# Kernel tuning notes

Measured on AMD Instinct MI355X. Metric: run time of the kernel, lower is better.

Reference implementation:

```python
import jax, jax.numpy as jnp
import numpy as np

NEG_SLOPE = 0.01  # torch LeakyReLU default
BN_EPS = 1e-5     # torch BatchNorm1d default


def _bn(x, g, b):
    # training-mode batch norm over the node axis
    m = jnp.mean(x, axis=0)
    v = jnp.var(x, axis=0)
    return g * (x - m) * jax.lax.rsqrt(v + BN_EPS) + b


def _lrelu(x):
    return jax.nn.leaky_relu(x, NEG_SLOPE)


def setup_inputs() -> dict:
    key = jax.random.key(0)
    N, E, W, D = 100_000, 1_600_000, 32, 10
    ks = iter(jax.random.split(key, 64))

    def w(shape):
        fan_in = shape[-2] if len(shape) >= 2 else shape[-1]
        return (jax.random.normal(next(ks), shape, jnp.float32) / np.sqrt(fan_in)).astype(jnp.float32)

    inp = {}
    inp["x"] = jax.random.normal(next(ks), (N, 1), jnp.float32)
    inp["col_e_idx"] = jax.random.randint(next(ks), (2, E), 0, N, dtype=jnp.int32)
    # init_node_feature_trans: MLP 1 -> [32] -> 32, LeakyReLU, batch_norm=True
    inp["Wi0"] = w((1, W)); inp["bi0"] = jnp.zeros(W); inp["gi0"] = jnp.ones(W); inp["bei0"] = jnp.zeros(W)
    inp["Wi1"] = w((W, W)); inp["bi1"] = jnp.zeros(W); inp["gi1"] = jnp.ones(W); inp["bei1"] = jnp.zeros(W)
    # 10 CollConv layers (identical dims -> stacked params)
    inp["Wm"] = w((D, W, W)); inp["bm"] = jnp.zeros((D, W)); inp["gm"] = jnp.ones((D, W)); inp["bem"] = jnp.zeros((D, W))
    inp["Wu"] = w((D, 2 * W, W)); inp["bu"] = jnp.zeros((D, W)); inp["gu"] = jnp.ones((D, W)); inp["beu"] = jnp.zeros((D, W))
    # final_mlp: 32 -> 256 -> 128 -> 64 -> 32 (LeakyReLU, no BN), then 32 -> 1 sigmoid
    inp["Wf0"] = w((W, 256)); inp["bf0"] = jnp.zeros(256)
    inp["Wf1"] = w((256, 128)); inp["bf1"] = jnp.zeros(128)
    inp["Wf2"] = w((128, 64)); inp["bf2"] = jnp.zeros(64)
    inp["Wf3"] = w((64, W)); inp["bf3"] = jnp.zeros(W)
    inp["Wo"] = w((W, 1)); inp["bo"] = jnp.zeros(1)
    return inp


def reference(x, col_e_idx, Wi0, bi0, gi0, bei0, Wi1, bi1, gi1, bei1,
              Wm, bm, gm, bem, Wu, bu, gu, beu,
              Wf0, bf0, Wf1, bf1, Wf2, bf2, Wf3, bf3, Wo, bo):
    N = x.shape[0]
    D = Wm.shape[0]
    src, dst = col_e_idx[0], col_e_idx[1]

    # init node-feature MLP (Linear -> BN -> LeakyReLU, twice)
    h = _lrelu(_bn(x @ Wi0 + bi0, gi0, bei0))
    h = _lrelu(_bn(h @ Wi1 + bi1, gi1, bei1))

    feats = [h]  # middle_features[0]
    for i in range(D):  # fixed small depth -> python loop is fine
        # CollConv: node-wise message transform, edge gather, scatter-sum, update
        msg = _lrelu(_bn(h @ Wm[i] + bm[i], gm[i], bem[i]))      # [N, W]
        agg = jax.ops.segment_sum(msg[src], dst, num_segments=N)  # [N, W]
        h = _lrelu(_bn(jnp.concatenate([h, agg], axis=-1) @ Wu[i] + bu[i], gu[i], beu[i]))
        if i - 2 >= 0:  # residual_skip_num = 2
            h = h + feats[i - 2]
        feats.append(h)

    # final MLP (no BN) + sigmoid head
    h = _lrelu(h @ Wf0 + bf0)
    h = _lrelu(h @ Wf1 + bf1)
    h = _lrelu(h @ Wf2 + bf2)
    h = _lrelu(h @ Wf3 + bf3)
    return jax.nn.sigmoid(h @ Wo + bo)  # [N, 1]
```

## Files before the change

kernel.cpp:

```cpp
#include <hip/hip_runtime.h>
#include <hip/hip_bf16.h>

#define NN 100000
#define NEDGE 1600000
#define NV (NN*32)
#define NEG 0.01f
#define EPS 1e-5f
#define NBLK 391
#define NBKT 391
#define CHUNK 4096
#define NCBLK 391
#define DCAP 6144
#define STC 64
#define ST_STRIDE 4096
#define NGBLK 1563

#define OFF_STATS 0
#define STATS_F  (22*ST_STRIDE)
#define OFF_PA   STATS_F
#define OFF_PB   (OFF_PA + NV)
#define OFF_TACT (OFF_PB + NV)
#define OFF_MSGB (OFF_TACT + NV)
#define OFF_RING (OFF_MSGB + NV/2)
#define OFF_WF   (OFF_RING + 4*NV)
#define ARENA_F  (OFF_WF + 25600)

#define W0B 0
#define W1B 1024
#define W2B 5120
#define W3B 6144

__device__ __align__(16) float gA[ARENA_F];
__device__ int g_rowptr[NN + 1];
__device__ int g_csr[NEDGE];
__device__ int g_bin[NEDGE];
__device__ int g_bcnt[NBKT];
__device__ int g_boff[NBKT];
__device__ int g_btail[NBKT];

__device__ __forceinline__ float lrelu(float v) { return v > 0.f ? v : v * NEG; }
__device__ __forceinline__ unsigned short f2b(float v) {
    __hip_bfloat16 b = __float2bfloat16(v);
    return *reinterpret_cast<unsigned short*>(&b);
}
__device__ __forceinline__ float b2f(unsigned short u) {
    __hip_bfloat16 b = *reinterpret_cast<__hip_bfloat16*>(&u);
    return __bfloat162float(b);
}

__global__ void k_zero_v19()
{
    int i = blockIdx.x * 256 + threadIdx.x;
    if (i < STATS_F) gA[i] = 0.f;
    if (i < NBKT) g_bcnt[i] = 0;
}

__global__ __launch_bounds__(256) void k_bcnt_v19(const int* __restrict__ col)
{
    __shared__ int hist[NBKT];
    int tid = threadIdx.x;
    for (int b = tid; b < NBKT; b += 256) hist[b] = 0;
    __syncthreads();
    int e0 = blockIdx.x * CHUNK;
    #pragma unroll
    for (int r = 0; r < CHUNK / 256; ++r) {
        int e = e0 + r * 256 + tid;
        if (e < NEDGE) atomicAdd(&hist[col[NEDGE + e] >> 8], 1);
    }
    __syncthreads();
    for (int b = tid; b < NBKT; b += 256) {
        int v = hist[b];
        if (v) atomicAdd(&g_bcnt[b], v);
    }
}

__global__ __launch_bounds__(512) void k_bscan_v19()
{
    __shared__ int s[512];
    int t = threadIdx.x;
    int v = (t < NBKT) ? g_bcnt[t] : 0;
    s[t] = v;
    __syncthreads();
    for (int off = 1; off < 512; off <<= 1) {
        int u = (t >= off) ? s[t - off] : 0;
        __syncthreads();
        s[t] += u;
        __syncthreads();
    }
    if (t < NBKT) {
        int o = s[t] - v;
        g_boff[t] = o;
        g_btail[t] = o;
    }
}

__global__ __launch_bounds__(256) void k_binfill_v19(const int* __restrict__ col)
{
    __shared__ int ssrc[CHUNK];
    __shared__ int sdst[CHUNK];
    __shared__ int hist[NBKT];
    __shared__ int boffL[NBKT];
    __shared__ int cnt2[NBKT];
    int tid = threadIdx.x;
    for (int b = tid; b < NBKT; b += 256) { hist[b] = 0; cnt2[b] = 0; }
    __syncthreads();
    int e0 = blockIdx.x * CHUNK;
    #pragma unroll
    for (int r = 0; r < CHUNK / 256; ++r) {
        int i = r * 256 + tid;
        int e = e0 + i;
        if (e < NEDGE) {
            int s = col[e];
            int d = col[NEDGE + e];
            ssrc[i] = s;
            sdst[i] = d;
            atomicAdd(&hist[d >> 8], 1);
        }
    }
    __syncthreads();
    for (int b = tid; b < NBKT; b += 256) {
        int h = hist[b];
        if (h) boffL[b] = atomicAdd(&g_btail[b], h);
    }
    __syncthreads();
    #pragma unroll
    for (int r = 0; r < CHUNK / 256; ++r) {
        int i = r * 256 + tid;
        int e = e0 + i;
        if (e < NEDGE) {
            int d = sdst[i];
            int b = d >> 8;
            int rk = atomicAdd(&cnt2[b], 1);
            g_bin[boffL[b] + rk] = (ssrc[i] << 8) | (d & 255);
        }
    }
}

__global__ __launch_bounds__(256) void k_csr_v21()
{
    __shared__ int stg[DCAP];
    __shared__ int srt[DCAP];
    __shared__ int c1[256];
    __shared__ int sc[256];
    __shared__ int sl[256];
    __shared__ int c2[256];
    int tid = threadIdx.x, b = blockIdx.x;
    int base = g_boff[b];
    int cntE = g_bcnt[b];
    c1[tid] = 0; c2[tid] = 0;
    __syncthreads();
    for (int i = tid; i < cntE; i += 256) {
        int p = g_bin[base + i];
        if (i < DCAP) stg[i] = p;
        atomicAdd(&c1[p & 255], 1);
    }
    __syncthreads();
    int v = c1[tid];
    sc[tid] = v;
    __syncthreads();
    for (int off = 1; off < 256; off <<= 1) {
        int u = (tid >= off) ? sc[tid - off] : 0;
        __syncthreads();
        sc[tid] += u;
        __syncthreads();
    }
    int loff = sc[tid] - v;
    sl[tid] = loff;
    int node = b * 256 + tid;
    if (node < NN) g_rowptr[node] = base + loff;
    if (b == NBKT - 1 && tid == 0) g_rowptr[NN] = NEDGE;
    __syncthreads();
    if (cntE <= DCAP) {
        for (int i = tid; i < cntE; i += 256) {
            int p = stg[i];
            int dl = p & 255;
            int rk = atomicAdd(&c2[dl], 1);
            srt[sl[dl] + rk] = p;
        }
        __syncthreads();
        int cnt = v;
        int s0 = loff;
        for (int i = 1; i < cnt; ++i) {
            int key = srt[s0 + i];
            int j = i - 1;
            while (j >= 0 && srt[s0 + j] > key) { srt[s0 + j + 1] = srt[s0 + j]; --j; }
            srt[s0 + j + 1] = key;
        }
        __syncthreads();
        for (int i = tid; i < cntE; i += 256)
            g_csr[base + i] = srt[i] >> 8;
    } else {
        for (int i = tid; i < cntE; i += 256) {
            int p = (i < DCAP) ? stg[i] : g_bin[base + i];
            int dl = p & 255;
            int rk = atomicAdd(&c2[dl], 1);
            g_csr[base + sl[dl] + rk] = p >> 8;
        }
    }
}

__global__ void k_init0_v17(const float* __restrict__ x, const float* __restrict__ Wi0,
                            const float* __restrict__ bi0)
{
    int j = threadIdx.x & 31, ns = threadIdx.x >> 5;
    float w = Wi0[j];
    float bb = bi0[j];
    __shared__ float red[64];
    if (threadIdx.x < 64) red[threadIdx.x] = 0.f;
    __syncthreads();
    float s1 = 0.f, s2 = 0.f;
    for (int t = blockIdx.x; t < NN / 8; t += gridDim.x) {
        int n = t * 8 + ns;
        float v = x[n] * w + bb;
        gA[OFF_PA + n * 32 + j] = v;
        s1 += v; s2 += v * v;
    }
    atomicAdd(&red[j], s1);
    atomicAdd(&red[j + 32], s2);
    __syncthreads();
    if (threadIdx.x < 64)
        atomicAdd(&gA[OFF_STATS + (blockIdx.x & (STC - 1)) * 64 + threadIdx.x], red[threadIdx.x]);
}

__global__ void k_nl_v17(int off_in, int off_out, int out_msg, int st_in,
                         const float* __restrict__ gamma, const float* __restrict__ beta,
                         int off_resid, int off_feats,
                         const float* __restrict__ Wn, const float* __restrict__ bn,
                         int st_out)
{
    int j = threadIdx.x & 31, ns = threadIdx.x >> 5;
    __shared__ float sstat[64];
    __shared__ float red[64];
    if (threadIdx.x < 64) {
        red[threadIdx.x] = 0.f;
        float acc = 0.f;
        int base = st_in + threadIdx.x;
        #pragma unroll 8
        for (int c = 0; c < STC; ++c) acc += gA[base + c * 64];
        sstat[threadIdx.x] = acc;
    }
    __syncthreads();
    float mean = sstat[j] * (1.f / NN);
    float var  = sstat[32 + j] * (1.f / NN) - mean * mean;
    float scale = gamma[j] * rsqrtf(var + EPS);
    float shift = beta[j] - mean * scale;

    float wc[32]; float bb = 0.f;
    if (Wn) {
        #pragma unroll
        for (int k = 0; k < 32; ++k) wc[k] = Wn[k * 32 + j];
        bb = bn[j];
    }
    unsigned short* mb = (unsigned short*)(gA + OFF_MSGB);
    __shared__ float sH[8][32];
    float s1 = 0.f, s2 = 0.f;
    for (int t = blockIdx.x; t < NN / 8; t += gridDim.x) {
        int n = t * 8 + ns;
        float v = gA[off_in + n * 32 + j];
        v = lrelu(scale * v + shift);
        if (off_resid >= 0) v += gA[off_resid + n * 32 + j];
        if (off_feats >= 0) gA[off_feats + n * 32 + j] = v;
        if (Wn) {
            sH[ns][j] = v;
            __syncthreads();
            float acc = bb;
            #pragma unroll
            for (int k = 0; k < 32; k += 4) {
                float4 h4 = *(const float4*)&sH[ns][k];
                acc += h4.x * wc[k] + h4.y * wc[k + 1] + h4.z * wc[k + 2] + h4.w * wc[k + 3];
            }
            if (out_msg) mb[n * 32 + j] = f2b(acc);
            else gA[off_out + n * 32 + j] = acc;
            s1 += acc; s2 += acc * acc;
            __syncthreads();
        }
    }
    if (Wn) {
        atomicAdd(&red[j], s1);
        atomicAdd(&red[j + 32], s2);
        __syncthreads();
        if (threadIdx.x < 64)
            atomicAdd(&gA[st_out + (blockIdx.x & (STC - 1)) * 64 + threadIdx.x], red[threadIdx.x]);
    }
}

__global__ __launch_bounds__(256) void k_act_v21(int st_msg,
                                                 const float* __restrict__ gm,
                                                 const float* __restrict__ bem)
{
    __shared__ float sstat[64];
    __shared__ float scl[32], shf[32];
    int tid = threadIdx.x;
    if (tid < 64) {
        float acc = 0.f;
        int base = st_msg + tid;
        #pragma unroll 8
        for (int c = 0; c < STC; ++c) acc += gA[base + c * 64];
        sstat[tid] = acc;
    }
    __syncthreads();
    if (tid < 32) {
        float mean = sstat[tid] * (1.f / NN);
        float var  = sstat[32 + tid] * (1.f / NN) - mean * mean;
        float s = gm[tid] * rsqrtf(var + EPS);
        scl[tid] = s;
        shf[tid] = bem[tid] - mean * s;
    }
    __syncthreads();
    int idx = blockIdx.x * 256 + tid;
    if (idx >= NV / 8) return;
    const uint4* src = (const uint4*)(gA + OFF_MSGB);
    uint4* dst = (uint4*)(gA + OFF_TACT);
    uint4 m = src[idx];
    int fb = (idx & 3) * 8;
    uint4 o;
    #pragma unroll
    for (int w = 0; w < 4; ++w) {
        unsigned int u = (&m.x)[w];
        int f0 = fb + 2 * w;
        float vlo = lrelu(scl[f0]     * __uint_as_float(u << 16)         + shf[f0]);
        float vhi = lrelu(scl[f0 + 1] * __uint_as_float(u & 0xffff0000u) + shf[f0 + 1]);
        (&o.x)[w] = (unsigned int)f2b(vlo) | ((unsigned int)f2b(vhi) << 16);
    }
    dst[idx] = o;
}

__global__ __launch_bounds__(256) void k_gupd_v21(int off_h,
                                                  const float* __restrict__ Wu_i,
                                                  const float* __restrict__ bu_i,
                                                  int st_out)
{
    __shared__ float sH[64][36];
    __shared__ float sAgg[64][36];
    __shared__ float red[64];
    int tid = threadIdx.x;
    int nb = blockIdx.x * 64;

    if (tid < 64) red[tid] = 0.f;
    {
        const float* hp = gA + off_h + nb * 32;
        int lim = min(2048, (NN - nb) * 32);
        for (int idx = tid; idx < lim; idx += 256)
            sH[idx >> 5][idx & 31] = hp[idx];
    }

    {
        int nl = tid >> 2;
        int g  = tid & 3;
        int n  = nb + nl;
        float a[8];
        #pragma unroll
        for (int q = 0; q < 8; ++q) a[q] = 0.f;
        if (n < NN) {
            const unsigned short* tb = (const unsigned short*)(gA + OFF_TACT);
            int e0 = g_rowptr[n], e1 = g_rowptr[n + 1];
            int e = e0;
            for (; e + 3 < e1; e += 4) {
                int sg = g_csr[e + g];
                int s0 = __shfl(sg, 0, 4);
                int s1 = __shfl(sg, 1, 4);
                int s2 = __shfl(sg, 2, 4);
                int s3 = __shfl(sg, 3, 4);
                uint4 m0 = *(const uint4*)(tb + (s0 << 5) + (g << 3));
                uint4 m1 = *(const uint4*)(tb + (s1 << 5) + (g << 3));
                uint4 m2 = *(const uint4*)(tb + (s2 << 5) + (g << 3));
                uint4 m3 = *(const uint4*)(tb + (s3 << 5) + (g << 3));
                #pragma unroll
                for (int w = 0; w < 4; ++w) {
                    unsigned int u0 = (&m0.x)[w], u1 = (&m1.x)[w], u2 = (&m2.x)[w], u3 = (&m3.x)[w];
                    int q = w * 2;
                    a[q]   += __uint_as_float(u0 << 16) + __uint_as_float(u1 << 16)
                            + __uint_as_float(u2 << 16) + __uint_as_float(u3 << 16);
                    a[q+1] += __uint_as_float(u0 & 0xffff0000u) + __uint_as_float(u1 & 0xffff0000u)
                            + __uint_as_float(u2 & 0xffff0000u) + __uint_as_float(u3 & 0xffff0000u);
                }
            }
            for (; e < e1; ++e) {
                int s0 = g_csr[e];
                uint4 m0 = *(const uint4*)(tb + (s0 << 5) + (g << 3));
                #pragma unroll
                for (int w = 0; w < 4; ++w) {
                    unsigned int u0 = (&m0.x)[w];
                    int q = w * 2;
                    a[q]   += __uint_as_float(u0 << 16);
                    a[q+1] += __uint_as_float(u0 & 0xffff0000u);
                }
            }
        }
        *(float4*)&sAgg[nl][g * 8]     = make_float4(a[0], a[1], a[2], a[3]);
        *(float4*)&sAgg[nl][g * 8 + 4] = make_float4(a[4], a[5], a[6], a[7]);
    }
    __syncthreads();

    {
        int j = tid & 31, ns = tid >> 5;
        float wc[64];
        #pragma unroll
        for (int k = 0; k < 64; ++k) wc[k] = Wu_i[k * 32 + j];
        float bb = bu_i[j];
        float s1 = 0.f, s2 = 0.f;
        #pragma unroll
        for (int it = 0; it < 8; ++it) {
            int nl = it * 8 + ns;
            int n = nb + nl;
            if (n >= NN) break;
            float acc = bb;
            #pragma unroll
            for (int k = 0; k < 32; k += 4) {
                float4 h4 = *(const float4*)&sH[nl][k];
                acc += h4.x * wc[k] + h4.y * wc[k + 1] + h4.z * wc[k + 2] + h4.w * wc[k + 3];
                float4 a4 = *(const float4*)&sAgg[nl][k];
                acc += a4.x * wc[32 + k] + a4.y * wc[32 + k + 1] + a4.z * wc[32 + k + 2] + a4.w * wc[32 + k + 3];
            }
            gA[OFF_PB + n * 32 + j] = acc;
            s1 += acc; s2 += acc * acc;
        }
        atomicAdd(&red[j], s1);
        atomicAdd(&red[j + 32], s2);
        __syncthreads();
        if (tid < 64)
            atomicAdd(&gA[st_out + (blockIdx.x & (STC - 1)) * 64 + tid], red[tid]);
    }
}

typedef __attribute__((ext_vector_type(8))) short bf16x8;
typedef __attribute__((ext_vector_type(4))) float f32x4;

union FC { uint4 u; bf16x8 b; };

#define MFMA(a, b, c) __builtin_amdgcn_mfma_f32_16x16x32_bf16(a, b, c, 0, 0, 0)

__device__ __forceinline__ bf16x8 ld_wf(const uint4* p) {
    FC c; c.u = *p; return c.b;
}

__device__ __forceinline__ f32x4 ld_bias4(const float* p) {
    float4 t = *(const float4*)p;
    f32x4 r; r[0] = t.x; r[1] = t.y; r[2] = t.z; r[3] = t.w; return r;
}

__device__ __forceinline__ f32x4 lrelu4(f32x4 v) {
    f32x4 r;
    #pragma unroll
    for (int k = 0; k < 4; ++k) r[k] = v[k] > 0.f ? v[k] : v[k] * NEG;
    return r;
}

__device__ __forceinline__ void splitpack(const float* v, bf16x8& hi, bf16x8& lo) {
    unsigned int h[4], l[4];
    #pragma unroll
    for (int k = 0; k < 4; ++k) {
        unsigned short h0 = f2b(v[2*k]), h1 = f2b(v[2*k+1]);
        float r0 = v[2*k]   - b2f(h0);
        float r1 = v[2*k+1] - b2f(h1);
        h[k] = (unsigned int)h0 | ((unsigned int)h1 << 16);
        l[k] = (unsigned int)f2b(r0) | ((unsigned int)f2b(r1) << 16);
    }
    FC ch; ch.u = make_uint4(h[0], h[1], h[2], h[3]); hi = ch.b;
    FC cl; cl.u = make_uint4(l[0], l[1], l[2], l[3]); lo = cl.b;
}

__global__ __launch_bounds__(256) void k_wprep_v18(const float* __restrict__ W0,
                                                   const float* __restrict__ W1,
                                                   const float* __restrict__ W2,
                                                   const float* __restrict__ W3)
{
    int i = blockIdx.x * 256 + threadIdx.x;
    if (i >= 51200) return;
    const float* src; int Nout, nk; int r = i;
    if (r < 8192)       { src = W0; Nout = 256; nk = 1; }
    else if (r < 40960) { src = W1; Nout = 128; nk = 8; r -= 8192; }
    else if (r < 49152) { src = W2; Nout = 64;  nk = 4; r -= 40960; }
    else                { src = W3; Nout = 32;  nk = 2; r -= 49152; }
    int frag = r >> 9;
    int lane = (r >> 3) & 63;
    int j = r & 7;
    int T = frag / nk, s = frag - T * nk;
    int g = lane >> 4;
    int outf = T * 16 + (lane & 15);
    int inf = 32 * s + 16 * (j >> 2) + 4 * g + (j & 3);
    unsigned short* dst = (unsigned short*)(gA + OFF_WF);
    dst[i] = f2b(src[inf * Nout + outf]);
}

__global__ __launch_bounds__(256) void k_final_v18(
    int off_h,
    const float* __restrict__ bf0, const float* __restrict__ bf1,
    const float* __restrict__ bf2, const float* __restrict__ bf3,
    const float* __restrict__ Wo,  const float* __restrict__ bo,
    float* __restrict__ out)
{
    int lane = threadIdx.x & 63;
    int wave = threadIdx.x >> 6;
    int c = lane & 15;
    int g = lane >> 4;
    int nb = blockIdx.x * 128 + wave * 32;
    int n0 = nb + c;
    int n1 = nb + 16 + c;
    int ld0 = min(n0, NN - 1), ld1 = min(n1, NN - 1);

    const float* h = gA + off_h;
    const uint4* WF = (const uint4*)(gA + OFF_WF);

    float4 ia0 = *(const float4*)&h[ld0 * 32 + 4 * g];
    float4 ib0 = *(const float4*)&h[ld0 * 32 + 16 + 4 * g];
    float4 ia1 = *(const float4*)&h[ld1 * 32 + 4 * g];
    float4 ib1 = *(const float4*)&h[ld1 * 32 + 16 + 4 * g];
    bf16x8 Bh0, Bl0, Bh1, Bl1;
    {
        float v0[8] = {ia0.x, ia0.y, ia0.z, ia0.w, ib0.x, ib0.y, ib0.z, ib0.w};
        float v1[8] = {ia1.x, ia1.y, ia1.z, ia1.w, ib1.x, ib1.y, ib1.z, ib1.w};
        splitpack(v0, Bh0, Bl0);
        splitpack(v1, Bh1, Bl1);
    }

    f32x4 A0[16][2];
    #pragma unroll
    for (int t = 0; t < 16; ++t) {
        f32x4 ci = ld_bias4(bf0 + t * 16 + 4 * g);
        bf16x8 w = ld_wf(WF + W0B + t * 64 + lane);
        f32x4 d0 = MFMA(w, Bh0, ci);
        d0 = MFMA(w, Bl0, d0);
        f32x4 d1 = MFMA(w, Bh1, ci);
        d1 = MFMA(w, Bl1, d1);
        A0[t][0] = lrelu4(d0);
        A0[t][1] = lrelu4(d1);
    }

    f32x4 A1[8][2];
    #pragma unroll
    for (int T = 0; T < 8; ++T) {
        f32x4 ci = ld_bias4(bf1 + T * 16 + 4 * g);
        A1[T][0] = ci; A1[T][1] = ci;
    }
    #pragma unroll
    for (int s = 0; s < 8; ++s) {
        bf16x8 bh[2], bl[2];
        #pragma unroll
        for (int u = 0; u < 2; ++u) {
            float vv[8] = {A0[2*s][u][0], A0[2*s][u][1], A0[2*s][u][2], A0[2*s][u][3],
                           A0[2*s+1][u][0], A0[2*s+1][u][1], A0[2*s+1][u][2], A0[2*s+1][u][3]};
            splitpack(vv, bh[u], bl[u]);
        }
        #pragma unroll
        for (int T = 0; T < 8; ++T) {
            bf16x8 w = ld_wf(WF + W1B + (T * 8 + s) * 64 + lane);
            A1[T][0] = MFMA(w, bh[0], A1[T][0]);
            A1[T][0] = MFMA(w, bl[0], A1[T][0]);
            A1[T][1] = MFMA(w, bh[1], A1[T][1]);
            A1[T][1] = MFMA(w, bl[1], A1[T][1]);
        }
    }
    #pragma unroll
    for (int T = 0; T < 8; ++T) { A1[T][0] = lrelu4(A1[T][0]); A1[T][1] = lrelu4(A1[T][1]); }

    f32x4 A2[4][2];
    #pragma unroll
    for (int T = 0; T < 4; ++T) {
        f32x4 ci = ld_bias4(bf2 + T * 16 + 4 * g);
        A2[T][0] = ci; A2[T][1] = ci;
    }
    #pragma unroll
    for (int s = 0; s < 4; ++s) {
        bf16x8 bh[2], bl[2];
        #pragma unroll
        for (int u = 0; u < 2; ++u) {
            float vv[8] = {A1[2*s][u][0], A1[2*s][u][1], A1[2*s][u][2], A1[2*s][u][3],
                           A1[2*s+1][u][0], A1[2*s+1][u][1], A1[2*s+1][u][2], A1[2*s+1][u][3]};
            splitpack(vv, bh[u], bl[u]);
        }
        #pragma unroll
        for (int T = 0; T < 4; ++T) {
            bf16x8 w = ld_wf(WF + W2B + (T * 4 + s) * 64 + lane);
            A2[T][0] = MFMA(w, bh[0], A2[T][0]);
            A2[T][0] = MFMA(w, bl[0], A2[T][0]);
            A2[T][1] = MFMA(w, bh[1], A2[T][1]);
            A2[T][1] = MFMA(w, bl[1], A2[T][1]);
        }
    }
    #pragma unroll
    for (int T = 0; T < 4; ++T) { A2[T][0] = lrelu4(A2[T][0]); A2[T][1] = lrelu4(A2[T][1]); }

    f32x4 A3[2][2];
    #pragma unroll
    for (int T = 0; T < 2; ++T) {
        f32x4 ci = ld_bias4(bf3 + T * 16 + 4 * g);
        A3[T][0] = ci; A3[T][1] = ci;
    }
    #pragma unroll
    for (int s = 0; s < 2; ++s) {
        bf16x8 bh[2], bl[2];
        #pragma unroll
        for (int u = 0; u < 2; ++u) {
            float vv[8] = {A2[2*s][u][0], A2[2*s][u][1], A2[2*s][u][2], A2[2*s][u][3],
                           A2[2*s+1][u][0], A2[2*s+1][u][1], A2[2*s+1][u][2], A2[2*s+1][u][3]};
            splitpack(vv, bh[u], bl[u]);
        }
        #pragma unroll
        for (int T = 0; T < 2; ++T) {
            bf16x8 w = ld_wf(WF + W3B + (T * 2 + s) * 64 + lane);
            A3[T][0] = MFMA(w, bh[0], A3[T][0]);
            A3[T][0] = MFMA(w, bl[0], A3[T][0]);
            A3[T][1] = MFMA(w, bh[1], A3[T][1]);
            A3[T][1] = MFMA(w, bl[1], A3[T][1]);
        }
    }
    #pragma unroll
    for (int T = 0; T < 2; ++T) { A3[T][0] = lrelu4(A3[T][0]); A3[T][1] = lrelu4(A3[T][1]); }

    float4 woa = *(const float4*)&Wo[4 * g];
    float4 wob = *(const float4*)&Wo[16 + 4 * g];
    float z0 = A3[0][0][0]*woa.x + A3[0][0][1]*woa.y + A3[0][0][2]*woa.z + A3[0][0][3]*woa.w
             + A3[1][0][0]*wob.x + A3[1][0][1]*wob.y + A3[1][0][2]*wob.z + A3[1][0][3]*wob.w;
    float z1 = A3[0][1][0]*woa.x + A3[0][1][1]*woa.y + A3[0][1][2]*woa.z + A3[0][1][3]*woa.w
             + A3[1][1][0]*wob.x + A3[1][1][1]*wob.y + A3[1][1][2]*wob.z + A3[1][1][3]*wob.w;
    z0 += __shfl_xor(z0, 16); z0 += __shfl_xor(z0, 32);
    z1 += __shfl_xor(z1, 16); z1 += __shfl_xor(z1, 32);
    float bb = bo[0];
    if (g == 0 && n0 < NN) out[n0] = 1.f / (1.f + __expf(-(z0 + bb)));
    if (g == 1 && n1 < NN) out[n1] = 1.f / (1.f + __expf(-(z1 + bb)));
}

extern "C" void kernel_launch(void* const* d_in, const int* in_sizes, int n_in,
                              void* d_out, int out_size, void* d_ws, size_t ws_size,
                              hipStream_t stream)
{
    (void)in_sizes; (void)n_in; (void)out_size; (void)d_ws; (void)ws_size;
    float* out = (float*)d_out;

    const float* x   = (const float*)d_in[0];
    const int*  col  = (const int*) d_in[1];
    const float* Wi0 = (const float*)d_in[2];
    const float* bi0 = (const float*)d_in[3];
    const float* gi0 = (const float*)d_in[4];
    const float* bei0= (const float*)d_in[5];
    const float* Wi1 = (const float*)d_in[6];
    const float* bi1 = (const float*)d_in[7];
    const float* gi1 = (const float*)d_in[8];
    const float* bei1= (const float*)d_in[9];
    const float* Wm  = (const float*)d_in[10];
    const float* bm  = (const float*)d_in[11];
    const float* gm  = (const float*)d_in[12];
    const float* bem = (const float*)d_in[13];
    const float* Wu  = (const float*)d_in[14];
    const float* bu  = (const float*)d_in[15];
    const float* gu  = (const float*)d_in[16];
    const float* beu = (const float*)d_in[17];
    const float* Wf0 = (const float*)d_in[18];
    const float* bf0 = (const float*)d_in[19];
    const float* Wf1 = (const float*)d_in[20];
    const float* bf1 = (const float*)d_in[21];
    const float* Wf2 = (const float*)d_in[22];
    const float* bf2 = (const float*)d_in[23];
    const float* Wf3 = (const float*)d_in[24];
    const float* bf3 = (const float*)d_in[25];
    const float* Wo  = (const float*)d_in[26];
    const float* bo  = (const float*)d_in[27];

    const int st_i0 = OFF_STATS;
    const int st_i1 = OFF_STATS + ST_STRIDE;
    const int st_m  = OFF_STATS + 2 * ST_STRIDE;
    const int st_u  = OFF_STATS + 12 * ST_STRIDE;

    const int RING[4] = { OFF_RING, OFF_RING + NV, OFF_RING + 2 * NV, OFF_RING + 3 * NV };

    dim3 blk(256);
    k_zero_v19<<<NBLK, blk, 0, stream>>>();
    k_bcnt_v19<<<NCBLK, blk, 0, stream>>>(col);
    k_bscan_v19<<<1, 512, 0, stream>>>();
    k_binfill_v19<<<NCBLK, blk, 0, stream>>>(col);
    k_csr_v21<<<NBKT, blk, 0, stream>>>();
    k_wprep_v18<<<200, blk, 0, stream>>>(Wf0, Wf1, Wf2, Wf3);

    k_init0_v17<<<1024, blk, 0, stream>>>(x, Wi0, bi0);
    k_nl_v17<<<1024, blk, 0, stream>>>(OFF_PA, OFF_PB, 0, st_i0, gi0, bei0, -1, -1, Wi1, bi1, st_i1);
    k_nl_v17<<<1024, blk, 0, stream>>>(OFF_PB, 0, 1, st_i1, gi1, bei1, -1, RING[0], Wm, bm, st_m);

    for (int i = 0; i < 10; ++i) {
        int h_cur = RING[i & 3];
        int h_new = RING[(i + 1) & 3];
        int resid = (i >= 2) ? RING[(i - 2) & 3] : -1;
        k_act_v21<<<1563, blk, 0, stream>>>(st_m + i * ST_STRIDE, gm + i * 32, bem + i * 32);
        k_gupd_v21<<<NGBLK, blk, 0, stream>>>(h_cur, Wu + i * 2048, bu + i * 32,
                                              st_u + i * ST_STRIDE);
        const float* Wn = (i < 9) ? (Wm + (i + 1) * 1024) : nullptr;
        const float* bn = (i < 9) ? (bm + (i + 1) * 32) : nullptr;
        int st_next = (i < 9) ? (st_m + (i + 1) * ST_STRIDE) : 0;
        k_nl_v17<<<1024, blk, 0, stream>>>(OFF_PB, 0, 1, st_u + i * ST_STRIDE,
                                           gu + i * 32, beu + i * 32,
                                           resid, h_new, Wn, bn, st_next);
    }

    k_final_v18<<<782, blk, 0, stream>>>(RING[2], bf0, bf1, bf2, bf3, Wo, bo, out);
}
```

Baseline: 988.6 us.

## Partition CSR rows by source quarter and gather in block-synchronised segments

The CSR build drops the per-row insertion sort. It buckets each destination's edges into four coarse source-index ranges using the top bits of the packed key, and stores the segment offsets per node in a new array. The gather kernel walks the four segments in order with a block-wide barrier after each, so all threads touch the same quarter of the message table at once, which aims to improve cache locality of the random gathers. The cost is extra barriers that make fast rows wait for slow ones. Edges within a segment are no longer sorted, so the fp32 summation order changes.

```diff
diff --git a/kernel.cpp b/kernel.cpp
--- a/kernel.cpp
+++ b/kernel.cpp
@@ -32,6 +32,7 @@
 
 __device__ __align__(16) float gA[ARENA_F];
 __device__ int g_rowptr[NN + 1];
+__device__ unsigned int g_segp[NN];
 __device__ int g_csr[NEDGE];
 __device__ int g_bin[NEDGE];
 __device__ int g_bcnt[NBKT];
@@ -136,27 +137,33 @@
     }
 }
 
-__global__ __launch_bounds__(256) void k_csr_v21()
+__global__ __launch_bounds__(256) void k_csr_v22()
 {
     __shared__ int stg[DCAP];
-    __shared__ int srt[DCAP];
-    __shared__ int c1[256];
+    __shared__ int c1[1024];
+    __shared__ int sgb[1024];
+    __shared__ int c2[1024];
     __shared__ int sc[256];
     __shared__ int sl[256];
-    __shared__ int c2[256];
     int tid = threadIdx.x, b = blockIdx.x;
     int base = g_boff[b];
     int cntE = g_bcnt[b];
-    c1[tid] = 0; c2[tid] = 0;
+    #pragma unroll
+    for (int k = 0; k < 4; ++k) { c1[tid + 256 * k] = 0; c2[tid + 256 * k] = 0; }
     __syncthreads();
     for (int i = tid; i < cntE; i += 256) {
         int p = g_bin[base + i];
         if (i < DCAP) stg[i] = p;
-        atomicAdd(&c1[p & 255], 1);
-    }
-    __syncthreads();
-    int v = c1[tid];
-    sc[tid] = v;
+        atomicAdd(&c1[((p & 255) << 2) | (p >> 23)], 1);
+    }
+    __syncthreads();
+    int t0 = c1[tid * 4], t1 = c1[tid * 4 + 1], t2 = c1[tid * 4 + 2], t3 = c1[tid * 4 + 3];
+    int deg = t0 + t1 + t2 + t3;
+    sgb[tid * 4]     = 0;
+    sgb[tid * 4 + 1] = t0;
+    sgb[tid * 4 + 2] = t0 + t1;
+    sgb[tid * 4 + 3] = t0 + t1 + t2;
+    sc[tid] = deg;
     __syncthreads();
     for (int off = 1; off < 256; off <<= 1) {
         int u = (tid >= off) ? sc[tid - off] : 0;
@@ -164,38 +171,22 @@
         sc[tid] += u;
         __syncthreads();
     }
-    int loff = sc[tid] - v;
+    int loff = sc[tid] - deg;
     sl[tid] = loff;
     int node = b * 256 + tid;
-    if (node < NN) g_rowptr[node] = base + loff;
+    if (node < NN) {
+        g_rowptr[node] = base + loff;
+        g_segp[node] = (unsigned int)t0 | ((unsigned int)(t0 + t1) << 8)
+                     | ((unsigned int)(t0 + t1 + t2) << 16);
+    }
     if (b == NBKT - 1 && tid == 0) g_rowptr[NN] = NEDGE;
     __syncthreads();
-    if (cntE <= DCAP) {
-        for (int i = tid; i < cntE; i += 256) {
-            int p = stg[i];
-            int dl = p & 255;
-            int rk = atomicAdd(&c2[dl], 1);
-            srt[sl[dl] + rk] = p;
-        }
-        __syncthreads();
-        int cnt = v;
-        int s0 = loff;
-        for (int i = 1; i < cnt; ++i) {
-            int key = srt[s0 + i];
-            int j = i - 1;
-            while (j >= 0 && srt[s0 + j] > key) { srt[s0 + j + 1] = srt[s0 + j]; --j; }
-            srt[s0 + j + 1] = key;
-        }
-        __syncthreads();
-        for (int i = tid; i < cntE; i += 256)
-            g_csr[base + i] = srt[i] >> 8;
-    } else {
-        for (int i = tid; i < cntE; i += 256) {
-            int p = (i < DCAP) ? stg[i] : g_bin[base + i];
-            int dl = p & 255;
-            int rk = atomicAdd(&c2[dl], 1);
-            g_csr[base + sl[dl] + rk] = p >> 8;
-        }
+    for (int i = tid; i < cntE; i += 256) {
+        int p = (i < DCAP) ? stg[i] : g_bin[base + i];
+        int dl = p & 255;
+        int key = (dl << 2) | (p >> 23);
+        int rk = atomicAdd(&c2[key], 1);
+        g_csr[base + sl[dl] + sgb[key] + rk] = p >> 8;
     }
 }
 
@@ -325,7 +316,7 @@
     dst[idx] = o;
 }
 
-__global__ __launch_bounds__(256) void k_gupd_v21(int off_h,
+__global__ __launch_bounds__(256) void k_gupd_v22(int off_h,
                                                   const float* __restrict__ Wu_i,
                                                   const float* __restrict__ bu_i,
                                                   int st_out)
@@ -351,11 +342,23 @@
         float a[8];
         #pragma unroll
         for (int q = 0; q < 8; ++q) a[q] = 0.f;
+        const unsigned short* tb = (const unsigned short*)(gA + OFF_TACT);
+        int qb[5];
         if (n < NN) {
-            const unsigned short* tb = (const unsigned short*)(gA + OFF_TACT);
             int e0 = g_rowptr[n], e1 = g_rowptr[n + 1];
-            int e = e0;
-            for (; e + 3 < e1; e += 4) {
+            unsigned int sp = g_segp[n];
+            qb[0] = e0;
+            qb[1] = e0 + (int)(sp & 255u);
+            qb[2] = e0 + (int)((sp >> 8) & 255u);
+            qb[3] = e0 + (int)((sp >> 16) & 255u);
+            qb[4] = e1;
+        } else {
+            qb[0] = qb[1] = qb[2] = qb[3] = qb[4] = 0;
+        }
+        #pragma unroll
+        for (int seg = 0; seg < 4; ++seg) {
+            int e = qb[seg], end = qb[seg + 1];
+            for (; e + 3 < end; e += 4) {
                 int sg = g_csr[e + g];
                 int s0 = __shfl(sg, 0, 4);
                 int s1 = __shfl(sg, 1, 4);
@@ -375,7 +378,7 @@
                             + __uint_as_float(u2 & 0xffff0000u) + __uint_as_float(u3 & 0xffff0000u);
                 }
             }
-            for (; e < e1; ++e) {
+            for (; e < end; ++e) {
                 int s0 = g_csr[e];
                 uint4 m0 = *(const uint4*)(tb + (s0 << 5) + (g << 3));
                 #pragma unroll
@@ -386,6 +389,7 @@
                     a[q+1] += __uint_as_float(u0 & 0xffff0000u);
                 }
             }
+            __syncthreads();
         }
         *(float4*)&sAgg[nl][g * 8]     = make_float4(a[0], a[1], a[2], a[3]);
         *(float4*)&sAgg[nl][g * 8 + 4] = make_float4(a[4], a[5], a[6], a[7]);
@@ -669,7 +673,7 @@
     k_bcnt_v19<<<NCBLK, blk, 0, stream>>>(col);
     k_bscan_v19<<<1, 512, 0, stream>>>();
     k_binfill_v19<<<NCBLK, blk, 0, stream>>>(col);
-    k_csr_v21<<<NBKT, blk, 0, stream>>>();
+    k_csr_v22<<<NBKT, blk, 0, stream>>>();
     k_wprep_v18<<<200, blk, 0, stream>>>(Wf0, Wf1, Wf2, Wf3);
 
     k_init0_v17<<<1024, blk, 0, stream>>>(x, Wi0, bi0);
@@ -681,7 +685,7 @@
         int h_new = RING[(i + 1) & 3];
         int resid = (i >= 2) ? RING[(i - 2) & 3] : -1;
         k_act_v21<<<1563, blk, 0, stream>>>(st_m + i * ST_STRIDE, gm + i * 32, bem + i * 32);
-        k_gupd_v21<<<NGBLK, blk, 0, stream>>>(h_cur, Wu + i * 2048, bu + i * 32,
+        k_gupd_v22<<<NGBLK, blk, 0, stream>>>(h_cur, Wu + i * 2048, bu + i * 32,
                                               st_u + i * ST_STRIDE);
         const float* Wn = (i < 9) ? (Wm + (i + 1) * 1024) : nullptr;
         const float* bn = (i < 9) ? (bm + (i + 1) * 32) : nullptr;
```

After: 1.018 ms. 2.9% more time.
